# Kernel tuning notes

Hardware: AMD Instinct MI355X
Metric: run time of the kernel (lower is better)

Reference implementation:

```python
import jax, jax.numpy as jnp
import numpy as np

R, STEPS, INJECT = 8, 4, 0.1


def _rmsnorm(v, w, eps=1e-6):
    return v * jax.lax.rsqrt(jnp.mean(v * v, axis=-1, keepdims=True) + eps) * w


def _layernorm(v, eps=1e-5):
    m = jnp.mean(v, axis=-1, keepdims=True)
    c = v - m
    return c * jax.lax.rsqrt(jnp.mean(c * c, axis=-1, keepdims=True) + eps)


def setup_inputs() -> dict:
    key = jax.random.key(0)
    ks = jax.random.split(key, 32)
    D, H, B, L = 1024, 256, 32, 2048
    s = 0.02
    inp = {
        'x': jax.random.normal(ks[0], (B, L, D), jnp.float32),
        'u': jax.random.uniform(ks[1], (STEPS, B, 16), jnp.float32),
        'W_e1': s * jax.random.normal(ks[2], (D, H)), 'b_e1': jnp.zeros((H,)),
        'W_e2': s * jax.random.normal(ks[3], (H, R * D)), 'b_e2': jnp.zeros((R * D,)),
        'W_ih': s * jax.random.normal(ks[4], (D + R * D, 3 * H)), 'b_ih': jnp.zeros((3 * H,)),
        'W_hh': s * jax.random.normal(ks[5], (H, 3 * H)), 'b_hh': jnp.zeros((3 * H,)),
        'ctrl_h0': jnp.zeros((H,)),
        'W_op': s * jax.random.normal(ks[6], (H, 16)), 'b_op': jnp.zeros((16,)),
        'W_src': s * jax.random.normal(ks[7], (H, R)), 'b_src': jnp.zeros((R,)),
        'W_dst': s * jax.random.normal(ks[8], (H, R)), 'b_dst': jnp.zeros((R,)),
        'W_aux': s * jax.random.normal(ks[9], (H, R)), 'b_aux': jnp.zeros((R,)),
        'W_proj': s * jax.random.normal(ks[10], (D, D)),
        'op_scale': jnp.ones((1,)),
        'Wv': s * jax.random.normal(ks[11], (D, D)), 'bv': jnp.zeros((D,)),
        'Wo': s * jax.random.normal(ks[12], (D, D)), 'bo': jnp.zeros((D,)),
        'W_d1': s * jax.random.normal(ks[13], (R * D, H)), 'b_d1': jnp.zeros((H,)),
        'W_d2': s * jax.random.normal(ks[14], (H, D)), 'b_d2': jnp.zeros((D,)),
        'norm_w': jnp.ones((D,)),
    }
    return inp


def reference(x, u, W_e1, b_e1, W_e2, b_e2, W_ih, b_ih, W_hh, b_hh, ctrl_h0,
              W_op, b_op, W_src, b_src, W_dst, b_dst, W_aux, b_aux,
              W_proj, op_scale, Wv, bv, Wo, bo, W_d1, b_d1, W_d2, b_d2, norm_w):
    B, L, D = x.shape
    pooled = x.mean(1)                                             # [B,D]
    regs = (jax.nn.gelu(pooled @ W_e1 + b_e1, approximate=False) @ W_e2 + b_e2).reshape(B, R, D)
    h = jnp.broadcast_to(ctrl_h0, (B, ctrl_h0.shape[0]))
    halt = jnp.zeros((B, 1), x.dtype)
    gumbel = -jnp.log(-jnp.log(u + 1e-20) + 1e-20)                 # [STEPS,B,16]
    op_trace = []
    for s in range(STEPS):
        ci = jnp.concatenate([pooled, regs.reshape(B, -1)], -1)    # [B, D+R*D]
        gi = ci @ W_ih + b_ih
        gh = h @ W_hh + b_hh
        ir, iz, inn = jnp.split(gi, 3, -1)
        hr, hz, hn = jnp.split(gh, 3, -1)
        r = jax.nn.sigmoid(ir + hr)
        z = jax.nn.sigmoid(iz + hz)
        n = jnp.tanh(inn + r * hn)
        h = (1.0 - z) * n + z * h                                  # GRUCell
        op_w = jax.nn.softmax(h @ W_op + b_op + gumbel[s], -1)     # gumbel-softmax, tau=1, soft
        src_w = jax.nn.softmax(h @ W_src + b_src, -1)
        dst_w = jax.nn.softmax(h @ W_dst + b_dst, -1)
        aux_w = jax.nn.softmax(h @ W_aux + b_aux, -1)
        src = jnp.einsum('br,brd->bd', src_w, regs)
        dst = jnp.einsum('br,brd->bd', dst_w, regs)
        aux = jnp.einsum('br,brd->bd', aux_w, regs)
        halt = halt + op_w[:, 15:16]
        live = jnp.clip(1.0 - halt, 0.0, None)
        # seq-len-1 MHA: softmax over one key == 1 -> out_proj(v_proj(aux))
        attn_out = (aux @ Wv + bv) @ Wo + bo
        results = jnp.stack([
            dst,                               # 0 NOP
            dst + src,                         # 1 ADD
            jax.nn.sigmoid(src) * dst,         # 2 GATE
            _layernorm(src),                   # 3 NORM
            src @ W_proj,                      # 4 PROJ
            src + dst,                         # 5 RESIDUAL
            attn_out,                          # 6 ATTEND
            -src,                              # 7 NEGATE
            src * op_scale,                    # 8 SCALE
            src,                               # 9 SWAP (as written)
            jnp.maximum(src, dst),             # 10 MAX
            jnp.minimum(src, dst),             # 11 MIN
            jax.nn.relu(src),                  # 12 RELU
            jnp.tanh(src),                     # 13 TANH
            (src * dst) @ W_proj,              # 14 OUTER
            dst,                               # 15 HALT
        ], axis=1)                             # [B,16,D]
        result = jnp.einsum('bo,bod->bd', op_w, results)
        regs = regs + dst_w[:, :, None] * (result * live)[:, None, :]
        op_trace.append(jnp.argmax(op_w, -1))
    prog_out = jax.nn.gelu(regs.reshape(B, -1) @ W_d1 + b_d1, approximate=False) @ W_d2 + b_d2
    prog_out = _rmsnorm(prog_out, norm_w)
    x_prog = _rmsnorm(x + prog_out[:, None, :] * INJECT, norm_w)
    return x_prog, regs, prog_out, jnp.stack(op_trace, axis=1)
```

## Files before the change

kernel.cpp:

```cpp
#include <hip/hip_runtime.h>
#include <math.h>
#include <stddef.h>

#define BB 32
#define LL 2048
#define DD 1024
#define HH 256
#define NSTEPS 4
#define RD 8192
#define G3 768

#define OUT_REGS 67108864UL
#define OUT_PO   67371008UL
#define OUT_TR   67403776UL

#define MM_KC 128
#define ATS 516

__device__ __forceinline__ float sigf(float x){ return 1.0f/(1.0f+expf(-x)); }
__device__ __forceinline__ float geluf(float x){ return x*0.5f*(1.0f+erff(x*0.70710678118654752f)); }

union SMem {
  struct { float At[8*ATS]; float Wt[MM_KC*64]; } mm;
  struct { float A[64*68]; float B[64*64]; } w2;
  struct { float hnew[HH]; float logit[40]; float wsm[40]; } ctl;
  struct { float p[DD]; } pool;
  struct { float ow[16]; float dw[8]; float redS[4]; float redQ[4]; float stats[2]; } comb;
  struct { float d1[HH]; float redQ[4]; float stats[1]; } dec;
};

struct MegaP {
  const float *x, *u, *W_e1, *b_e1, *W_e2, *b_e2, *W_ih, *b_ih, *W_hh, *b_hh, *h0;
  const float *W_op, *b_op, *W_src, *b_src, *W_dst, *b_dst, *W_aux, *b_aux;
  const float *W_proj, *op_sc, *Wv, *bv, *Wo, *bo, *W_d1, *b_d1, *W_d2, *b_d2, *norm_w;
  float *pool_part, *pooled, *e1, *regs, *gip_part, *gi_part, *ghpart, *hbuf, *halt;
  float *opw, *dstw, *live, *srcv, *dstv, *tvec, *avec, *p8a, *p10, *d1part, *pn;
  float *W2, *bvWo;
  float *out;
};

__device__ void st_mm2(SMem& sm, const float* __restrict__ in, int in_ld,
                       const float* __restrict__ W, int row_off, int ldw,
                       float* __restrict__ part, int nb, int layer, int nk, int t){
  float acc[16];
  #pragma unroll
  for (int i=0;i<16;++i) acc[i]=0.f;
  const int n0 = nb*64;
  for (int c=0;c<nk;++c){
    const int k0 = (layer*nk + c)*MM_KC;
    __syncthreads();
    if (t < 128){
      #pragma unroll
      for (int rep=0; rep<8; ++rep){
        int idx = t + rep*128;
        int b = idx & 31, k4 = idx >> 5;
        float4 g = *(const float4*)(in + (size_t)b*in_ld + k0 + k4*4);
        float* a = sm.mm.At + (b>>2)*ATS + k4*16 + (b&3);
        a[0]=g.x; a[4]=g.y; a[8]=g.z; a[12]=g.w;
      }
      #pragma unroll
      for (int rep=0; rep<16; ++rep){
        int idx = t + rep*128;
        int k = idx >> 4, nq4 = idx & 15;
        *(float4*)(sm.mm.Wt + k*64 + nq4*4) =
          *(const float4*)(W + (size_t)(row_off + k0 + k)*ldw + n0 + nq4*4);
      }
    }
    __syncthreads();
    if (t < 128){
      const int nq = t & 15, bq = t >> 4;
      const float4* A4 = (const float4*)sm.mm.At + bq*129;
      const float4* W4 = (const float4*)sm.mm.Wt + nq;
      #pragma unroll 4
      for (int kk=0; kk<MM_KC; ++kk){
        float4 a = A4[kk];
        float4 w = W4[kk*16];
        acc[0] +=a.x*w.x; acc[1] +=a.x*w.y; acc[2] +=a.x*w.z; acc[3] +=a.x*w.w;
        acc[4] +=a.y*w.x; acc[5] +=a.y*w.y; acc[6] +=a.y*w.z; acc[7] +=a.y*w.w;
        acc[8] +=a.z*w.x; acc[9] +=a.z*w.y; acc[10]+=a.z*w.z; acc[11]+=a.z*w.w;
        acc[12]+=a.w*w.x; acc[13]+=a.w*w.y; acc[14]+=a.w*w.z; acc[15]+=a.w*w.w;
      }
    }
  }
  if (t < 128){
    const int nq = t & 15, bq = t >> 4;
    float* pp = part + (size_t)(layer*32 + bq*4)*ldw + n0 + nq*4;
    #pragma unroll
    for (int i=0;i<4;++i){
      float4 o; o.x=acc[i*4]; o.y=acc[i*4+1]; o.z=acc[i*4+2]; o.w=acc[i*4+3];
      *(float4*)(pp + (size_t)i*ldw) = o;
    }
  }
}

__device__ void st_w2(SMem& sm, const MegaP& P, int blk, int t){
  const int r0 = (blk>>4)*64, n0 = (blk&15)*64;
  const int tr = t>>4, tc = t&15;
  float4 acc[4];
  acc[0]=make_float4(0,0,0,0); acc[1]=make_float4(0,0,0,0);
  acc[2]=make_float4(0,0,0,0); acc[3]=make_float4(0,0,0,0);
  for (int kc=0; kc<16; ++kc){
    const int k0 = kc*64;
    __syncthreads();
    #pragma unroll
    for (int rep=0; rep<4; ++rep){
      int idx = t + rep*256;
      int r = idx>>4, c4 = (idx&15)*4;
      *(float4*)(sm.w2.A + r*68 + c4) = *(const float4*)(P.Wv + (size_t)(r0+r)*DD + k0 + c4);
      *(float4*)(sm.w2.B + r*64 + c4) = *(const float4*)(P.Wo + (size_t)(k0+r)*DD + n0 + c4);
    }
    __syncthreads();
    #pragma unroll 4
    for (int k=0;k<64;++k){
      float4 bv4 = *(const float4*)(sm.w2.B + k*64 + tc*4);
      float a0 = sm.w2.A[(tr*4+0)*68 + k];
      float a1 = sm.w2.A[(tr*4+1)*68 + k];
      float a2 = sm.w2.A[(tr*4+2)*68 + k];
      float a3 = sm.w2.A[(tr*4+3)*68 + k];
      acc[0].x += a0*bv4.x; acc[0].y += a0*bv4.y; acc[0].z += a0*bv4.z; acc[0].w += a0*bv4.w;
      acc[1].x += a1*bv4.x; acc[1].y += a1*bv4.y; acc[1].z += a1*bv4.z; acc[1].w += a1*bv4.w;
      acc[2].x += a2*bv4.x; acc[2].y += a2*bv4.y; acc[2].z += a2*bv4.z; acc[2].w += a2*bv4.w;
      acc[3].x += a3*bv4.x; acc[3].y += a3*bv4.y; acc[3].z += a3*bv4.z; acc[3].w += a3*bv4.w;
    }
  }
  #pragma unroll
  for (int i=0;i<4;++i)
    *(float4*)(P.W2 + (size_t)(r0+tr*4+i)*DD + n0 + tc*4) = acc[i];
}

__global__ __launch_bounds__(256) void k_pool(MegaP P){
  const int blk = blockIdx.x, t = threadIdx.x;
  const int b = blk >> 5, c = blk & 31;
  const float* xp = P.x + (size_t)b*LL*DD + (size_t)c*64*DD + t*4;
  float ax=0.f, ay=0.f, az=0.f, aw=0.f;
  #pragma unroll 8
  for (int l=0;l<64;++l){
    float4 v = *(const float4*)(xp + (size_t)l*DD);
    ax+=v.x; ay+=v.y; az+=v.z; aw+=v.w;
  }
  float4 o; o.x=ax; o.y=ay; o.z=az; o.w=aw;
  *(float4*)(P.pool_part + (size_t)blk*DD + t*4) = o;
}

__global__ __launch_bounds__(256) void k_s1(MegaP P){
  __shared__ SMem sm;
  const int b = blockIdx.x, t = threadIdx.x;
  float ax=0.f, ay=0.f, az=0.f, aw=0.f;
  #pragma unroll 8
  for (int c=0;c<32;++c){
    float4 v = *(const float4*)(P.pool_part + (size_t)(b*32+c)*DD + t*4);
    ax+=v.x; ay+=v.y; az+=v.z; aw+=v.w;
  }
  const float inv = 1.0f/(float)LL;
  float4 o; o.x=ax*inv; o.y=ay*inv; o.z=az*inv; o.w=aw*inv;
  *(float4*)(P.pooled + (size_t)b*DD + t*4) = o;
  *(float4*)(sm.pool.p + t*4) = o;
  P.hbuf[b*HH + t] = P.h0[t];
  if (t==0) P.halt[b] = 0.f;
  __syncthreads();
  float a0=0.f,a1=0.f,a2=0.f,a3=0.f;
  #pragma unroll 2
  for (int k=0;k<DD;k+=4){
    a0 += sm.pool.p[k]  *P.W_e1[(k)*HH + t];
    a1 += sm.pool.p[k+1]*P.W_e1[(k+1)*HH + t];
    a2 += sm.pool.p[k+2]*P.W_e1[(k+2)*HH + t];
    a3 += sm.pool.p[k+3]*P.W_e1[(k+3)*HH + t];
  }
  float a = (a0+a1)+(a2+a3) + P.b_e1[t];
  P.e1[b*HH + t] = geluf(a);
}

__global__ __launch_bounds__(256) void k_s2(MegaP P){
  __shared__ SMem sm;
  const int blk = blockIdx.x, t = threadIdx.x;
  if (blk < 256){
    const int b = t>>3, cq = t&7;
    const int col = blk*32 + cq*4;
    float4 acc = *(const float4*)(P.b_e2 + col);
    const float* e1b = P.e1 + b*HH;
    const float* w = P.W_e2 + col;
    #pragma unroll 4
    for (int k=0;k<HH;++k){
      float ev = e1b[k];
      float4 wv = *(const float4*)(w + (size_t)k*RD);
      acc.x += ev*wv.x; acc.y += ev*wv.y; acc.z += ev*wv.z; acc.w += ev*wv.w;
    }
    *(float4*)(P.regs + (size_t)b*RD + col) = acc;
  } else if (blk < 352){
    const int i = blk - 256;
    st_mm2(sm, P.pooled, DD, P.W_ih, 0, G3, P.gip_part, i%12, i/12, 1, t);
  } else if (blk < 608){
    st_w2(sm, P, blk-352, t);
  } else if (blk < 612){
    const int col = (blk-608)*256 + t;
    float a = 0.f;
    #pragma unroll 8
    for (int j=0;j<DD;++j) a += P.bv[j]*P.Wo[(size_t)j*DD + col];
    P.bvWo[col] = a;
  } else {
    const int col = (blk-612)*256 + t;
    float a = 0.f;
    #pragma unroll 8
    for (int k=0;k<HH;++k) a += P.h0[k]*P.W_hh[(size_t)k*G3 + col];
    #pragma unroll
    for (int b=0;b<BB;++b) P.ghpart[b*G3 + col] = a;
  }
}

__global__ __launch_bounds__(128) void k_gi(MegaP P){
  __shared__ SMem sm;
  st_mm2(sm, P.regs, RD, P.W_ih, DD, G3, P.gi_part, blockIdx.x%12, blockIdx.x/12, 2, threadIdx.x);
}

__global__ __launch_bounds__(256) void k_control(MegaP P, int s){
  __shared__ SMem sm;
  const int b = blockIdx.x, t = threadIdx.x;
  const float hold = P.hbuf[b*HH + t];
  float gi[3], gh[3];
  #pragma unroll
  for (int j=0;j<3;++j){
    const int n = t + j*256;
    float a = P.b_ih[n];
    #pragma unroll
    for (int l=0;l<8;++l)  a += P.gip_part[(size_t)(l*BB+b)*G3 + n];
    #pragma unroll 8
    for (int l=0;l<32;++l) a += P.gi_part[(size_t)(l*BB+b)*G3 + n];
    gi[j] = a;
    gh[j] = P.b_hh[n] + P.ghpart[b*G3 + n];
  }
  {
    float r = sigf(gi[0]+gh[0]), z = sigf(gi[1]+gh[1]);
    float nn = tanhf(gi[2] + r*gh[2]);
    float hv = (1.0f - z)*nn + z*hold;
    sm.ctl.hnew[t] = hv;
    P.hbuf[b*HH + t] = hv;
  }
  __syncthreads();
  if (t < 40){
    const float* Wc; float bias; int col, ld;
    if (t < 16){ Wc=P.W_op; col=t; ld=16;
      float uu = P.u[s*BB*16 + b*16 + col];
      bias = P.b_op[col] + (-logf(-logf(uu + 1e-20f) + 1e-20f)); }
    else if (t<24){ Wc=P.W_src; col=t-16; ld=8; bias=P.b_src[col]; }
    else if (t<32){ Wc=P.W_dst; col=t-24; ld=8; bias=P.b_dst[col]; }
    else          { Wc=P.W_aux; col=t-32; ld=8; bias=P.b_aux[col]; }
    float a = bias;
    #pragma unroll 4
    for (int k=0;k<HH;++k) a += sm.ctl.hnew[k]*Wc[k*ld + col];
    sm.ctl.logit[t] = a;
  }
  __syncthreads();
  if (t == 0){
    float m = sm.ctl.logit[0]; int am = 0;
    for (int i=1;i<16;++i){ if (sm.ctl.logit[i] > m){ m = sm.ctl.logit[i]; am = i; } }
    float e[16]; float sum = 0.f;
    for (int i=0;i<16;++i){ e[i] = expf(sm.ctl.logit[i]-m); sum += e[i]; }
    float inv = 1.0f/sum;
    for (int i=0;i<16;++i){ float w = e[i]*inv; sm.ctl.wsm[i] = w; P.opw[b*16+i] = w; }
    float hl = P.halt[b] + sm.ctl.wsm[15];
    P.halt[b] = hl;
    P.live[b] = fmaxf(1.0f - hl, 0.0f);
    P.out[OUT_TR + b*NSTEPS + s] = (float)am;
  } else if (t <= 3){
    int base = 16 + (t-1)*8;
    float m = sm.ctl.logit[base];
    for (int i=1;i<8;++i) m = fmaxf(m, sm.ctl.logit[base+i]);
    float e[8]; float sum=0.f;
    for (int i=0;i<8;++i){ e[i]=expf(sm.ctl.logit[base+i]-m); sum+=e[i]; }
    float inv = 1.0f/sum;
    for (int i=0;i<8;++i){
      float w = e[i]*inv; sm.ctl.wsm[base+i] = w;
      if (t==2) P.dstw[b*8+i] = w;
    }
  }
  __syncthreads();
  {
    float w4 = sm.ctl.wsm[4], w14 = sm.ctl.wsm[14], w6 = sm.ctl.wsm[6];
    float sx=0,sy=0,sz=0,sw=0, dx=0,dy=0,dz=0,dw_=0, axx=0,ayy=0,azz=0,aww=0;
    #pragma unroll
    for (int r=0;r<8;++r){
      float ws = sm.ctl.wsm[16+r], wd = sm.ctl.wsm[24+r], wa = sm.ctl.wsm[32+r];
      float4 rv = *(const float4*)(P.regs + (size_t)b*RD + r*DD + t*4);
      sx += ws*rv.x; sy += ws*rv.y; sz += ws*rv.z; sw += ws*rv.w;
      dx += wd*rv.x; dy += wd*rv.y; dz += wd*rv.z; dw_ += wd*rv.w;
      axx += wa*rv.x; ayy += wa*rv.y; azz += wa*rv.z; aww += wa*rv.w;
    }
    float4 o;
    o.x=sx;o.y=sy;o.z=sz;o.w=sw;       *(float4*)(P.srcv + b*DD + t*4) = o;
    o.x=dx;o.y=dy;o.z=dz;o.w=dw_;      *(float4*)(P.dstv + b*DD + t*4) = o;
    o.x = w4*sx + w14*sx*dx;  o.y = w4*sy + w14*sy*dy;
    o.z = w4*sz + w14*sz*dz;  o.w = w4*sw + w14*sw*dw_;
    *(float4*)(P.tvec + b*DD + t*4) = o;
    o.x=w6*axx;o.y=w6*ayy;o.z=w6*azz;o.w=w6*aww;
    *(float4*)(P.avec + b*DD + t*4) = o;
  }
}

__global__ __launch_bounds__(128) void k_pv(MegaP P){
  __shared__ SMem sm;
  const int blk = blockIdx.x, t = threadIdx.x;
  if (blk < 128)       st_mm2(sm, P.tvec, DD, P.W_proj, 0, DD, P.p8a, blk>>3, blk&7, 1, t);
  else if (blk < 256){ int r = blk-128; st_mm2(sm, P.avec, DD, P.W2, 0, DD, P.p10, r>>3, r&7, 1, t); }
  else               { int r = blk-256; st_mm2(sm, P.hbuf, HH, P.W_hh, 0, G3, P.ghpart, r, 0, 2, t); }
}

__global__ __launch_bounds__(256) void k_combine(MegaP P){
  __shared__ SMem sm;
  const int b = blockIdx.x, t = threadIdx.x;
  if (t<16) sm.comb.ow[t] = P.opw[b*16+t];
  if (t<8)  sm.comb.dw[t] = P.dstw[b*8+t];
  float4 sv = *(const float4*)(P.srcv + b*DD + t*4);
  float4 dv = *(const float4*)(P.dstv + b*DD + t*4);
  float s1 = sv.x+sv.y+sv.z+sv.w;
  float s2 = sv.x*sv.x + sv.y*sv.y + sv.z*sv.z + sv.w*sv.w;
  #pragma unroll
  for (int off=32; off; off>>=1){ s1 += __shfl_xor(s1, off, 64); s2 += __shfl_xor(s2, off, 64); }
  if ((t&63)==0){ sm.comb.redS[t>>6]=s1; sm.comb.redQ[t>>6]=s2; }
  __syncthreads();
  if (t==0){
    float S = sm.comb.redS[0]+sm.comb.redS[1]+sm.comb.redS[2]+sm.comb.redS[3];
    float Q = sm.comb.redQ[0]+sm.comb.redQ[1]+sm.comb.redQ[2]+sm.comb.redQ[3];
    float mean = S*(1.0f/DD);
    float var = Q*(1.0f/DD) - mean*mean;
    sm.comb.stats[0]=mean; sm.comb.stats[1]=rsqrtf(var + 1e-5f);
  }
  __syncthreads();
  const float mean = sm.comb.stats[0], rstd = sm.comb.stats[1];
  const float live = P.live[b], osc = P.op_sc[0];
  float pmx=0,pmy=0,pmz=0,pmw=0, atx=0,aty=0,atz=0,atw=0;
  #pragma unroll
  for (int l=0;l<8;++l){
    float4 v = *(const float4*)(P.p8a + (size_t)(l*BB+b)*DD + t*4);
    pmx+=v.x; pmy+=v.y; pmz+=v.z; pmw+=v.w;
    float4 w = *(const float4*)(P.p10 + (size_t)(l*BB+b)*DD + t*4);
    atx+=w.x; aty+=w.y; atz+=w.z; atw+=w.w;
  }
  float4 bo4 = *(const float4*)(P.bo + t*4);
  float4 bw4 = *(const float4*)(P.bvWo + t*4);
  atx += sm.comb.ow[6]*(bo4.x + bw4.x); aty += sm.comb.ow[6]*(bo4.y + bw4.y);
  atz += sm.comb.ow[6]*(bo4.z + bw4.z); atw += sm.comb.ow[6]*(bo4.w + bw4.w);
  float S[4]={sv.x,sv.y,sv.z,sv.w}, Dv[4]={dv.x,dv.y,dv.z,dv.w};
  float PM[4]={pmx,pmy,pmz,pmw}, AT[4]={atx,aty,atz,atw};
  float rl[4];
  #pragma unroll
  for (int c=0;c<4;++c){
    float sc=S[c], dc=Dv[c];
    float r = sm.comb.ow[0]*dc + sm.comb.ow[1]*(dc+sc) + sm.comb.ow[2]*(sigf(sc)*dc)
            + sm.comb.ow[3]*((sc-mean)*rstd)
            + PM[c] + sm.comb.ow[5]*(sc+dc) + AT[c]
            - sm.comb.ow[7]*sc + sm.comb.ow[8]*(sc*osc) + sm.comb.ow[9]*sc
            + sm.comb.ow[10]*fmaxf(sc,dc) + sm.comb.ow[11]*fminf(sc,dc)
            + sm.comb.ow[12]*fmaxf(sc,0.0f)
            + sm.comb.ow[13]*tanhf(sc) + sm.comb.ow[15]*dc;
    rl[c] = r*live;
  }
  #pragma unroll
  for (int r=0;r<8;++r){
    float4* rp = (float4*)(P.regs + (size_t)b*RD + r*DD + t*4);
    float4 rv = *rp;
    rv.x += sm.comb.dw[r]*rl[0]; rv.y += sm.comb.dw[r]*rl[1];
    rv.z += sm.comb.dw[r]*rl[2]; rv.w += sm.comb.dw[r]*rl[3];
    *rp = rv;
  }
}

__global__ __launch_bounds__(128) void k_d1(MegaP P){
  __shared__ SMem sm;
  st_mm2(sm, P.regs, RD, P.W_d1, 0, HH, P.d1part, blockIdx.x&3, blockIdx.x>>2, 2, threadIdx.x);
}

__global__ __launch_bounds__(256) void k_decode(MegaP P){
  __shared__ SMem sm;
  const int b = blockIdx.x, t = threadIdx.x;
  float a = P.b_d1[t];
  #pragma unroll 8
  for (int l=0;l<32;++l) a += P.d1part[(size_t)(l*BB+b)*HH + t];
  sm.dec.d1[t] = geluf(a);
  __syncthreads();
  float4 acc = *(const float4*)(P.b_d2 + t*4);
  #pragma unroll 4
  for (int k=0;k<HH;++k){
    float4 w = *(const float4*)(P.W_d2 + (size_t)k*DD + t*4);
    float dk = sm.dec.d1[k];
    acc.x += dk*w.x; acc.y += dk*w.y; acc.z += dk*w.z; acc.w += dk*w.w;
  }
  float q = acc.x*acc.x + acc.y*acc.y + acc.z*acc.z + acc.w*acc.w;
  #pragma unroll
  for (int off=32; off; off>>=1) q += __shfl_xor(q, off, 64);
  if ((t&63)==0) sm.dec.redQ[t>>6]=q;
  __syncthreads();
  if (t==0) sm.dec.stats[0] = rsqrtf((sm.dec.redQ[0]+sm.dec.redQ[1]+sm.dec.redQ[2]+sm.dec.redQ[3])*(1.0f/DD) + 1e-6f);
  __syncthreads();
  const float rs = sm.dec.stats[0];
  float4 nw = *(const float4*)(P.norm_w + t*4);
  float4 po;
  po.x = acc.x*rs*nw.x; po.y = acc.y*rs*nw.y; po.z = acc.z*rs*nw.z; po.w = acc.w*rs*nw.w;
  *(float4*)(P.pn + (size_t)b*DD + t*4) = po;
  *(float4*)(P.out + OUT_PO + (size_t)b*DD + t*4) = po;
  const float4* rsrc = (const float4*)(P.regs + (size_t)b*RD);
  float4* rdst = (float4*)(P.out + OUT_REGS + (size_t)b*RD);
  for (int i=t;i<RD/4;i+=256) rdst[i] = rsrc[i];
}

__global__ __launch_bounds__(256) void k_xprog(
    const float* __restrict__ x, const float* __restrict__ pn,
    const float* __restrict__ norm_w, float* __restrict__ out)
{
  const int t = threadIdx.x;
  const int lane = t & 63;
  const int w = blockIdx.x*4 + (t>>6);
  const int row0 = w*4;
  const int b = row0 >> 11;
  float4 nw[4], pv[4];
  #pragma unroll
  for (int j=0;j<4;++j){
    nw[j] = *(const float4*)(norm_w + j*256 + lane*4);
    float4 p = *(const float4*)(pn + (size_t)b*DD + j*256 + lane*4);
    pv[j].x = 0.1f*p.x; pv[j].y = 0.1f*p.y; pv[j].z = 0.1f*p.z; pv[j].w = 0.1f*p.w;
  }
  #pragma unroll
  for (int r=0;r<4;++r){
    const int row = row0 + r;
    const float* xp = x + (size_t)row*DD;
    float4 y[4]; float ss = 0.f;
    #pragma unroll
    for (int j=0;j<4;++j){
      float4 xv = *(const float4*)(xp + j*256 + lane*4);
      y[j].x = xv.x + pv[j].x; y[j].y = xv.y + pv[j].y;
      y[j].z = xv.z + pv[j].z; y[j].w = xv.w + pv[j].w;
      ss += y[j].x*y[j].x + y[j].y*y[j].y + y[j].z*y[j].z + y[j].w*y[j].w;
    }
    #pragma unroll
    for (int off=32; off; off>>=1) ss += __shfl_xor(ss, off, 64);
    float rsd = rsqrtf(ss*(1.0f/DD) + 1e-6f);
    float* op = out + (size_t)row*DD;
    #pragma unroll
    for (int j=0;j<4;++j){
      float4 o;
      o.x=y[j].x*rsd*nw[j].x; o.y=y[j].y*rsd*nw[j].y;
      o.z=y[j].z*rsd*nw[j].z; o.w=y[j].w*rsd*nw[j].w;
      *(float4*)(op + j*256 + lane*4) = o;
    }
  }
}

extern "C" void kernel_launch(void* const* d_in, const int* in_sizes, int n_in,
                              void* d_out, int out_size, void* d_ws, size_t ws_size,
                              hipStream_t stream)
{
  (void)in_sizes; (void)n_in; (void)out_size; (void)ws_size;
  float* out = (float*)d_out;
  float* ws  = (float*)d_ws;

  size_t o = 0;
  float* pool_part = ws + o; o += 32UL*32*1024;
  float* pooled    = ws + o; o += 32UL*1024;
  float* e1        = ws + o; o += 32UL*256;
  float* regs      = ws + o; o += 32UL*8192;
  float* gip_part  = ws + o; o += 8UL*32*768;
  float* gi_part   = ws + o; o += 32UL*32*768;
  float* ghpart    = ws + o; o += 32UL*768;
  float* hbuf      = ws + o; o += 32UL*256;
  float* halt      = ws + o; o += 32;
  float* opw       = ws + o; o += 32*16;
  float* dstw      = ws + o; o += 32*8;
  float* live      = ws + o; o += 32;
  float* srcv      = ws + o; o += 32UL*1024;
  float* dstv      = ws + o; o += 32UL*1024;
  float* tvec      = ws + o; o += 32UL*1024;
  float* avec      = ws + o; o += 32UL*1024;
  float* p8a       = ws + o; o += 8UL*32*1024;
  float* p10       = ws + o; o += 8UL*32*1024;
  float* d1part    = ws + o; o += 32UL*32*256;
  float* pn        = ws + o; o += 32UL*1024;
  float* W2        = ws + o; o += 1024UL*1024;
  float* bvWo      = ws + o; o += 1024;

  MegaP P;
  P.x     = (const float*)d_in[0];
  P.u     = (const float*)d_in[1];
  P.W_e1  = (const float*)d_in[2];
  P.b_e1  = (const float*)d_in[3];
  P.W_e2  = (const float*)d_in[4];
  P.b_e2  = (const float*)d_in[5];
  P.W_ih  = (const float*)d_in[6];
  P.b_ih  = (const float*)d_in[7];
  P.W_hh  = (const float*)d_in[8];
  P.b_hh  = (const float*)d_in[9];
  P.h0    = (const float*)d_in[10];
  P.W_op  = (const float*)d_in[11];
  P.b_op  = (const float*)d_in[12];
  P.W_src = (const float*)d_in[13];
  P.b_src = (const float*)d_in[14];
  P.W_dst = (const float*)d_in[15];
  P.b_dst = (const float*)d_in[16];
  P.W_aux = (const float*)d_in[17];
  P.b_aux = (const float*)d_in[18];
  P.W_proj= (const float*)d_in[19];
  P.op_sc = (const float*)d_in[20];
  P.Wv    = (const float*)d_in[21];
  P.bv    = (const float*)d_in[22];
  P.Wo    = (const float*)d_in[23];
  P.bo    = (const float*)d_in[24];
  P.W_d1  = (const float*)d_in[25];
  P.b_d1  = (const float*)d_in[26];
  P.W_d2  = (const float*)d_in[27];
  P.b_d2  = (const float*)d_in[28];
  P.norm_w= (const float*)d_in[29];
  P.pool_part=pool_part; P.pooled=pooled; P.e1=e1; P.regs=regs;
  P.gip_part=gip_part; P.gi_part=gi_part; P.ghpart=ghpart; P.hbuf=hbuf; P.halt=halt;
  P.opw=opw; P.dstw=dstw; P.live=live; P.srcv=srcv; P.dstv=dstv;
  P.tvec=tvec; P.avec=avec; P.p8a=p8a; P.p10=p10; P.d1part=d1part; P.pn=pn;
  P.W2=W2; P.bvWo=bvWo; P.out=out;

  hipLaunchKernelGGL(k_pool, dim3(1024), dim3(256), 0, stream, P);
  hipLaunchKernelGGL(k_s1,   dim3(32),   dim3(256), 0, stream, P);
  hipLaunchKernelGGL(k_s2,   dim3(615),  dim3(256), 0, stream, P);
  for (int s=0;s<NSTEPS;++s){
    hipLaunchKernelGGL(k_gi,      dim3(384), dim3(128), 0, stream, P);
    hipLaunchKernelGGL(k_control, dim3(32),  dim3(256), 0, stream, P, s);
    hipLaunchKernelGGL(k_pv,      dim3(268), dim3(128), 0, stream, P);
    hipLaunchKernelGGL(k_combine, dim3(32),  dim3(256), 0, stream, P);
  }
  hipLaunchKernelGGL(k_d1,     dim3(128), dim3(128), 0, stream, P);
  hipLaunchKernelGGL(k_decode, dim3(32),  dim3(256), 0, stream, P);
  hipLaunchKernelGGL(k_xprog,  dim3(4096),dim3(256), 0, stream, P.x, pn, P.norm_w, out);
}
```

Measured before the change: 615.1 us.

## Fuse combine step into next GEMM's A-load via deferred register updates

Removes the per-step k_combine kernel. Each step's register update is stored as a rank-1 delta (rlbuf plus dst weights), and later kernels reconstruct regs on the fly: the gi GEMM, control, d1 GEMM and decode. LayerNorm statistics for src are moved into k_control. This cuts four launches and the read-modify-write of regs, but it adds redundant recomputation of the combine expression in every GEMM block that loads A tiles, plus extra loads of earlier deltas.

```diff
diff --git a/kernel.cpp b/kernel.cpp
--- a/kernel.cpp
+++ b/kernel.cpp
@@ -23,10 +23,10 @@
 union SMem {
   struct { float At[8*ATS]; float Wt[MM_KC*64]; } mm;
   struct { float A[64*68]; float B[64*64]; } w2;
-  struct { float hnew[HH]; float logit[40]; float wsm[40]; } ctl;
+  struct { float hnew[HH]; float logit[40]; float wsm[40]; float dws[32];
+           float redS[4]; float redQ[4]; } ctl;
   struct { float p[DD]; } pool;
-  struct { float ow[16]; float dw[8]; float redS[4]; float redQ[4]; float stats[2]; } comb;
-  struct { float d1[HH]; float redQ[4]; float stats[1]; } dec;
+  struct { float d1[HH]; float redQ[4]; float stats[1]; float dws[32]; } dec;
 };
 
 struct MegaP {
@@ -34,10 +34,46 @@
   const float *W_op, *b_op, *W_src, *b_src, *W_dst, *b_dst, *W_aux, *b_aux;
   const float *W_proj, *op_sc, *Wv, *bv, *Wo, *bo, *W_d1, *b_d1, *W_d2, *b_d2, *norm_w;
   float *pool_part, *pooled, *e1, *regs, *gip_part, *gi_part, *ghpart, *hbuf, *halt;
-  float *opw, *dstw, *live, *srcv, *dstv, *tvec, *avec, *p8a, *p10, *d1part, *pn;
+  float *opw, *live, *srcv, *dstv, *tvec, *avec, *p8a, *p10, *d1part, *pn;
   float *W2, *bvWo;
+  float *rlbuf, *dwbuf, *statsb;
   float *out;
 };
+
+__device__ __forceinline__ float4 rl_now4(const MegaP& P, int b, int d,
+    const float* ow, float live, float mean, float rstd, float osc){
+  float4 sv = *(const float4*)(P.srcv + (size_t)b*DD + d);
+  float4 dv = *(const float4*)(P.dstv + (size_t)b*DD + d);
+  float pmx=0,pmy=0,pmz=0,pmw=0, atx=0,aty=0,atz=0,atw=0;
+  #pragma unroll
+  for (int l=0;l<8;++l){
+    float4 v = *(const float4*)(P.p8a + (size_t)(l*BB+b)*DD + d);
+    pmx+=v.x; pmy+=v.y; pmz+=v.z; pmw+=v.w;
+    float4 w = *(const float4*)(P.p10 + (size_t)(l*BB+b)*DD + d);
+    atx+=w.x; aty+=w.y; atz+=w.z; atw+=w.w;
+  }
+  float4 bo4 = *(const float4*)(P.bo + d);
+  float4 bw4 = *(const float4*)(P.bvWo + d);
+  atx += ow[6]*(bo4.x+bw4.x); aty += ow[6]*(bo4.y+bw4.y);
+  atz += ow[6]*(bo4.z+bw4.z); atw += ow[6]*(bo4.w+bw4.w);
+  float S[4]={sv.x,sv.y,sv.z,sv.w}, Dv[4]={dv.x,dv.y,dv.z,dv.w};
+  float PM[4]={pmx,pmy,pmz,pmw}, AT[4]={atx,aty,atz,atw};
+  float R[4];
+  #pragma unroll
+  for (int c=0;c<4;++c){
+    float sc=S[c], dc=Dv[c];
+    float r = ow[0]*dc + ow[1]*(dc+sc) + ow[2]*(sigf(sc)*dc)
+            + ow[3]*((sc-mean)*rstd)
+            + PM[c] + ow[5]*(sc+dc) + AT[c]
+            - ow[7]*sc + ow[8]*(sc*osc) + ow[9]*sc
+            + ow[10]*fmaxf(sc,dc) + ow[11]*fminf(sc,dc)
+            + ow[12]*fmaxf(sc,0.0f)
+            + ow[13]*tanhf(sc) + ow[15]*dc;
+    R[c] = r*live;
+  }
+  float4 o; o.x=R[0]; o.y=R[1]; o.z=R[2]; o.w=R[3];
+  return o;
+}
 
 __device__ void st_mm2(SMem& sm, const float* __restrict__ in, int in_ld,
                        const float* __restrict__ W, int row_off, int ldw,
@@ -93,6 +129,89 @@
   }
 }
 
+__device__ void st_mm_regs(SMem& sm, const MegaP& P, int s_done,
+                           const float* __restrict__ W, int row_off, int ldw,
+                           float* __restrict__ part, int nb, int layer, int t, bool wr){
+  float acc[16];
+  #pragma unroll
+  for (int i=0;i<16;++i) acc[i]=0.f;
+  const int n0 = nb*64;
+  const int b = t & 31;
+  const int r_blk = layer >> 2;
+  float ow[16]; float live=0.f, mean=0.f, rstd=0.f, osc=0.f, dw_now=0.f;
+  float dw_prev[3] = {0.f,0.f,0.f};
+  if (s_done >= 1 && t < 128){
+    #pragma unroll
+    for (int i=0;i<16;++i) ow[i] = P.opw[b*16+i];
+    live = P.live[b]; mean = P.statsb[b*2]; rstd = P.statsb[b*2+1]; osc = P.op_sc[0];
+    dw_now = P.dwbuf[(size_t)(s_done-1)*256 + b*8 + r_blk];
+    #pragma unroll
+    for (int sp=0; sp<3; ++sp)
+      if (sp < s_done-1) dw_prev[sp] = P.dwbuf[(size_t)sp*256 + b*8 + r_blk];
+  }
+  for (int c=0;c<2;++c){
+    const int k0 = (layer*2 + c)*MM_KC;
+    __syncthreads();
+    if (t < 128){
+      #pragma unroll
+      for (int rep=0; rep<8; ++rep){
+        int idx = t + rep*128;
+        int k4 = idx >> 5;
+        int kq = k0 + k4*4;
+        int dq = kq & (DD-1);
+        float4 g = *(const float4*)(P.regs + (size_t)b*RD + kq);
+        #pragma unroll
+        for (int sp=0; sp<3; ++sp){
+          if (sp < s_done-1){
+            float4 rv = *(const float4*)(P.rlbuf + ((size_t)sp*BB + b)*DD + dq);
+            g.x += dw_prev[sp]*rv.x; g.y += dw_prev[sp]*rv.y;
+            g.z += dw_prev[sp]*rv.z; g.w += dw_prev[sp]*rv.w;
+          }
+        }
+        if (s_done >= 1){
+          float4 rn = rl_now4(P, b, dq, ow, live, mean, rstd, osc);
+          g.x += dw_now*rn.x; g.y += dw_now*rn.y;
+          g.z += dw_now*rn.z; g.w += dw_now*rn.w;
+          if (wr) *(float4*)(P.rlbuf + ((size_t)(s_done-1)*BB + b)*DD + dq) = rn;
+        }
+        float* a = sm.mm.At + (b>>2)*ATS + k4*16 + (b&3);
+        a[0]=g.x; a[4]=g.y; a[8]=g.z; a[12]=g.w;
+      }
+      #pragma unroll
+      for (int rep=0; rep<16; ++rep){
+        int idx = t + rep*128;
+        int k = idx >> 4, nq4 = idx & 15;
+        *(float4*)(sm.mm.Wt + k*64 + nq4*4) =
+          *(const float4*)(W + (size_t)(row_off + k0 + k)*ldw + n0 + nq4*4);
+      }
+    }
+    __syncthreads();
+    if (t < 128){
+      const int nq = t & 15, bq = t >> 4;
+      const float4* A4 = (const float4*)sm.mm.At + bq*129;
+      const float4* W4 = (const float4*)sm.mm.Wt + nq;
+      #pragma unroll 4
+      for (int kk=0; kk<MM_KC; ++kk){
+        float4 a = A4[kk];
+        float4 w = W4[kk*16];
+        acc[0] +=a.x*w.x; acc[1] +=a.x*w.y; acc[2] +=a.x*w.z; acc[3] +=a.x*w.w;
+        acc[4] +=a.y*w.x; acc[5] +=a.y*w.y; acc[6] +=a.y*w.z; acc[7] +=a.y*w.w;
+        acc[8] +=a.z*w.x; acc[9] +=a.z*w.y; acc[10]+=a.z*w.z; acc[11]+=a.z*w.w;
+        acc[12]+=a.w*w.x; acc[13]+=a.w*w.y; acc[14]+=a.w*w.z; acc[15]+=a.w*w.w;
+      }
+    }
+  }
+  if (t < 128){
+    const int nq = t & 15, bq = t >> 4;
+    float* pp = part + (size_t)(layer*32 + bq*4)*ldw + n0 + nq*4;
+    #pragma unroll
+    for (int i=0;i<4;++i){
+      float4 o; o.x=acc[i*4]; o.y=acc[i*4+1]; o.z=acc[i*4+2]; o.w=acc[i*4+3];
+      *(float4*)(pp + (size_t)i*ldw) = o;
+    }
+  }
+}
+
 __device__ void st_w2(SMem& sm, const MegaP& P, int blk, int t){
   const int r0 = (blk>>4)*64, n0 = (blk&15)*64;
   const int tr = t>>4, tc = t&15;
@@ -207,14 +326,20 @@
   }
 }
 
-__global__ __launch_bounds__(128) void k_gi(MegaP P){
+__global__ __launch_bounds__(128) void k_gic(MegaP P, int s){
   __shared__ SMem sm;
-  st_mm2(sm, P.regs, RD, P.W_ih, DD, G3, P.gi_part, blockIdx.x%12, blockIdx.x/12, 2, threadIdx.x);
+  const int nb = blockIdx.x%12, layer = blockIdx.x/12;
+  st_mm_regs(sm, P, s, P.W_ih, DD, G3, P.gi_part, nb, layer, threadIdx.x,
+             (nb==0 && layer<4));
 }
 
 __global__ __launch_bounds__(256) void k_control(MegaP P, int s){
   __shared__ SMem sm;
   const int b = blockIdx.x, t = threadIdx.x;
+  if (t < 32){
+    int sp = t>>3, r = t&7;
+    sm.ctl.dws[t] = (sp < s) ? P.dwbuf[(size_t)sp*256 + b*8 + r] : 0.f;
+  }
   const float hold = P.hbuf[b*HH + t];
   float gi[3], gh[3];
   #pragma unroll
@@ -270,17 +395,33 @@
     float inv = 1.0f/sum;
     for (int i=0;i<8;++i){
       float w = e[i]*inv; sm.ctl.wsm[base+i] = w;
-      if (t==2) P.dstw[b*8+i] = w;
+      if (t==2) P.dwbuf[(size_t)s*256 + b*8 + i] = w;
     }
   }
   __syncthreads();
+  float sx,sy,sz,sw;
   {
     float w4 = sm.ctl.wsm[4], w14 = sm.ctl.wsm[14], w6 = sm.ctl.wsm[6];
-    float sx=0,sy=0,sz=0,sw=0, dx=0,dy=0,dz=0,dw_=0, axx=0,ayy=0,azz=0,aww=0;
+    sx=0;sy=0;sz=0;sw=0;
+    float dx=0,dy=0,dz=0,dw_=0, axx=0,ayy=0,azz=0,aww=0;
+    float4 rlq[3];
+    #pragma unroll
+    for (int sp=0; sp<3; ++sp){
+      if (sp < s) rlq[sp] = *(const float4*)(P.rlbuf + ((size_t)sp*BB + b)*DD + t*4);
+      else { rlq[sp].x=0;rlq[sp].y=0;rlq[sp].z=0;rlq[sp].w=0; }
+    }
     #pragma unroll
     for (int r=0;r<8;++r){
       float ws = sm.ctl.wsm[16+r], wd = sm.ctl.wsm[24+r], wa = sm.ctl.wsm[32+r];
       float4 rv = *(const float4*)(P.regs + (size_t)b*RD + r*DD + t*4);
+      #pragma unroll
+      for (int sp=0; sp<3; ++sp){
+        if (sp < s){
+          float dwv = sm.ctl.dws[sp*8+r];
+          rv.x += dwv*rlq[sp].x; rv.y += dwv*rlq[sp].y;
+          rv.z += dwv*rlq[sp].z; rv.w += dwv*rlq[sp].w;
+        }
+      }
       sx += ws*rv.x; sy += ws*rv.y; sz += ws*rv.z; sw += ws*rv.w;
       dx += wd*rv.x; dy += wd*rv.y; dz += wd*rv.z; dw_ += wd*rv.w;
       axx += wa*rv.x; ayy += wa*rv.y; azz += wa*rv.z; aww += wa*rv.w;
@@ -294,6 +435,22 @@
     o.x=w6*axx;o.y=w6*ayy;o.z=w6*azz;o.w=w6*aww;
     *(float4*)(P.avec + b*DD + t*4) = o;
   }
+  {
+    float s1 = sx+sy+sz+sw;
+    float s2 = sx*sx + sy*sy + sz*sz + sw*sw;
+    #pragma unroll
+    for (int off=32; off; off>>=1){ s1 += __shfl_xor(s1, off, 64); s2 += __shfl_xor(s2, off, 64); }
+    if ((t&63)==0){ sm.ctl.redS[t>>6]=s1; sm.ctl.redQ[t>>6]=s2; }
+    __syncthreads();
+    if (t==0){
+      float S = sm.ctl.redS[0]+sm.ctl.redS[1]+sm.ctl.redS[2]+sm.ctl.redS[3];
+      float Q = sm.ctl.redQ[0]+sm.ctl.redQ[1]+sm.ctl.redQ[2]+sm.ctl.redQ[3];
+      float mean = S*(1.0f/DD);
+      float var = Q*(1.0f/DD) - mean*mean;
+      P.statsb[b*2]   = mean;
+      P.statsb[b*2+1] = rsqrtf(var + 1e-5f);
+    }
+  }
 }
 
 __global__ __launch_bounds__(128) void k_pv(MegaP P){
@@ -304,74 +461,17 @@
   else               { int r = blk-256; st_mm2(sm, P.hbuf, HH, P.W_hh, 0, G3, P.ghpart, r, 0, 2, t); }
 }
 
-__global__ __launch_bounds__(256) void k_combine(MegaP P){
-  __shared__ SMem sm;
-  const int b = blockIdx.x, t = threadIdx.x;
-  if (t<16) sm.comb.ow[t] = P.opw[b*16+t];
-  if (t<8)  sm.comb.dw[t] = P.dstw[b*8+t];
-  float4 sv = *(const float4*)(P.srcv + b*DD + t*4);
-  float4 dv = *(const float4*)(P.dstv + b*DD + t*4);
-  float s1 = sv.x+sv.y+sv.z+sv.w;
-  float s2 = sv.x*sv.x + sv.y*sv.y + sv.z*sv.z + sv.w*sv.w;
-  #pragma unroll
-  for (int off=32; off; off>>=1){ s1 += __shfl_xor(s1, off, 64); s2 += __shfl_xor(s2, off, 64); }
-  if ((t&63)==0){ sm.comb.redS[t>>6]=s1; sm.comb.redQ[t>>6]=s2; }
-  __syncthreads();
-  if (t==0){
-    float S = sm.comb.redS[0]+sm.comb.redS[1]+sm.comb.redS[2]+sm.comb.redS[3];
-    float Q = sm.comb.redQ[0]+sm.comb.redQ[1]+sm.comb.redQ[2]+sm.comb.redQ[3];
-    float mean = S*(1.0f/DD);
-    float var = Q*(1.0f/DD) - mean*mean;
-    sm.comb.stats[0]=mean; sm.comb.stats[1]=rsqrtf(var + 1e-5f);
-  }
-  __syncthreads();
-  const float mean = sm.comb.stats[0], rstd = sm.comb.stats[1];
-  const float live = P.live[b], osc = P.op_sc[0];
-  float pmx=0,pmy=0,pmz=0,pmw=0, atx=0,aty=0,atz=0,atw=0;
-  #pragma unroll
-  for (int l=0;l<8;++l){
-    float4 v = *(const float4*)(P.p8a + (size_t)(l*BB+b)*DD + t*4);
-    pmx+=v.x; pmy+=v.y; pmz+=v.z; pmw+=v.w;
-    float4 w = *(const float4*)(P.p10 + (size_t)(l*BB+b)*DD + t*4);
-    atx+=w.x; aty+=w.y; atz+=w.z; atw+=w.w;
-  }
-  float4 bo4 = *(const float4*)(P.bo + t*4);
-  float4 bw4 = *(const float4*)(P.bvWo + t*4);
-  atx += sm.comb.ow[6]*(bo4.x + bw4.x); aty += sm.comb.ow[6]*(bo4.y + bw4.y);
-  atz += sm.comb.ow[6]*(bo4.z + bw4.z); atw += sm.comb.ow[6]*(bo4.w + bw4.w);
-  float S[4]={sv.x,sv.y,sv.z,sv.w}, Dv[4]={dv.x,dv.y,dv.z,dv.w};
-  float PM[4]={pmx,pmy,pmz,pmw}, AT[4]={atx,aty,atz,atw};
-  float rl[4];
-  #pragma unroll
-  for (int c=0;c<4;++c){
-    float sc=S[c], dc=Dv[c];
-    float r = sm.comb.ow[0]*dc + sm.comb.ow[1]*(dc+sc) + sm.comb.ow[2]*(sigf(sc)*dc)
-            + sm.comb.ow[3]*((sc-mean)*rstd)
-            + PM[c] + sm.comb.ow[5]*(sc+dc) + AT[c]
-            - sm.comb.ow[7]*sc + sm.comb.ow[8]*(sc*osc) + sm.comb.ow[9]*sc
-            + sm.comb.ow[10]*fmaxf(sc,dc) + sm.comb.ow[11]*fminf(sc,dc)
-            + sm.comb.ow[12]*fmaxf(sc,0.0f)
-            + sm.comb.ow[13]*tanhf(sc) + sm.comb.ow[15]*dc;
-    rl[c] = r*live;
-  }
-  #pragma unroll
-  for (int r=0;r<8;++r){
-    float4* rp = (float4*)(P.regs + (size_t)b*RD + r*DD + t*4);
-    float4 rv = *rp;
-    rv.x += sm.comb.dw[r]*rl[0]; rv.y += sm.comb.dw[r]*rl[1];
-    rv.z += sm.comb.dw[r]*rl[2]; rv.w += sm.comb.dw[r]*rl[3];
-    *rp = rv;
-  }
-}
-
 __global__ __launch_bounds__(128) void k_d1(MegaP P){
   __shared__ SMem sm;
-  st_mm2(sm, P.regs, RD, P.W_d1, 0, HH, P.d1part, blockIdx.x&3, blockIdx.x>>2, 2, threadIdx.x);
+  const int nb = blockIdx.x & 3, layer = blockIdx.x >> 2;
+  st_mm_regs(sm, P, NSTEPS, P.W_d1, 0, HH, P.d1part, nb, layer, threadIdx.x,
+             (nb==0 && layer<4));
 }
 
 __global__ __launch_bounds__(256) void k_decode(MegaP P){
   __shared__ SMem sm;
   const int b = blockIdx.x, t = threadIdx.x;
+  if (t < 32) sm.dec.dws[t] = P.dwbuf[(size_t)(t>>3)*256 + b*8 + (t&7)];
   float a = P.b_d1[t];
   #pragma unroll 8
   for (int l=0;l<32;++l) a += P.d1part[(size_t)(l*BB+b)*HH + t];
@@ -399,7 +499,18 @@
   *(float4*)(P.out + OUT_PO + (size_t)b*DD + t*4) = po;
   const float4* rsrc = (const float4*)(P.regs + (size_t)b*RD);
   float4* rdst = (float4*)(P.out + OUT_REGS + (size_t)b*RD);
-  for (int i=t;i<RD/4;i+=256) rdst[i] = rsrc[i];
+  for (int i=t;i<RD/4;i+=256){
+    float4 v = rsrc[i];
+    const int r = i >> 8;
+    const int dq = (i & 255)*4;
+    #pragma unroll
+    for (int sp=0; sp<4; ++sp){
+      float4 rv = *(const float4*)(P.rlbuf + ((size_t)sp*BB + b)*DD + dq);
+      float dwv = sm.dec.dws[sp*8+r];
+      v.x += dwv*rv.x; v.y += dwv*rv.y; v.z += dwv*rv.z; v.w += dwv*rv.w;
+    }
+    rdst[i] = v;
+  }
 }
 
 __global__ __launch_bounds__(256) void k_xprog(
@@ -463,7 +574,6 @@
   float* hbuf      = ws + o; o += 32UL*256;
   float* halt      = ws + o; o += 32;
   float* opw       = ws + o; o += 32*16;
-  float* dstw      = ws + o; o += 32*8;
   float* live      = ws + o; o += 32;
   float* srcv      = ws + o; o += 32UL*1024;
   float* dstv      = ws + o; o += 32UL*1024;
@@ -475,6 +585,9 @@
   float* pn        = ws + o; o += 32UL*1024;
   float* W2        = ws + o; o += 1024UL*1024;
   float* bvWo      = ws + o; o += 1024;
+  float* rlbuf     = ws + o; o += 4UL*32*1024;
+  float* dwbuf     = ws + o; o += 4UL*32*8;
+  float* statsb    = ws + o; o += 64;
 
   MegaP P;
   P.x     = (const float*)d_in[0];
@@ -509,18 +622,17 @@
   P.norm_w= (const float*)d_in[29];
   P.pool_part=pool_part; P.pooled=pooled; P.e1=e1; P.regs=regs;
   P.gip_part=gip_part; P.gi_part=gi_part; P.ghpart=ghpart; P.hbuf=hbuf; P.halt=halt;
-  P.opw=opw; P.dstw=dstw; P.live=live; P.srcv=srcv; P.dstv=dstv;
+  P.opw=opw; P.live=live; P.srcv=srcv; P.dstv=dstv;
   P.tvec=tvec; P.avec=avec; P.p8a=p8a; P.p10=p10; P.d1part=d1part; P.pn=pn;
-  P.W2=W2; P.bvWo=bvWo; P.out=out;
+  P.W2=W2; P.bvWo=bvWo; P.rlbuf=rlbuf; P.dwbuf=dwbuf; P.statsb=statsb; P.out=out;
 
   hipLaunchKernelGGL(k_pool, dim3(1024), dim3(256), 0, stream, P);
   hipLaunchKernelGGL(k_s1,   dim3(32),   dim3(256), 0, stream, P);
   hipLaunchKernelGGL(k_s2,   dim3(615),  dim3(256), 0, stream, P);
   for (int s=0;s<NSTEPS;++s){
-    hipLaunchKernelGGL(k_gi,      dim3(384), dim3(128), 0, stream, P);
+    hipLaunchKernelGGL(k_gic,     dim3(384), dim3(128), 0, stream, P, s);
     hipLaunchKernelGGL(k_control, dim3(32),  dim3(256), 0, stream, P, s);
     hipLaunchKernelGGL(k_pv,      dim3(268), dim3(128), 0, stream, P);
-    hipLaunchKernelGGL(k_combine, dim3(32),  dim3(256), 0, stream, P);
   }
   hipLaunchKernelGGL(k_d1,     dim3(128), dim3(128), 0, stream, P);
   hipLaunchKernelGGL(k_decode, dim3(32),  dim3(256), 0, stream, P);
```

Result: slower. 790.2 us (+28.5%).
